# Kernel optimization log

Hardware: AMD Instinct MI355X
Metric: run time of the kernel (lower is better)

Reference implementation:

```python
import jax, jax.numpy as jnp
import numpy as np

N_NODES = 50000
N_EDGES = 800000
D_IN = 128
D_HID = 128
D_OUT = 128


def _gcn_layer(x, W, b, src, dst, norm):
    # dense projection then edge-weighted gather -> scatter-add at dst
    h = x @ W                                   # [N, d_out]
    msg = h[src] * norm[:, None]                # [E, d_out]
    out = jax.ops.segment_sum(msg, dst, num_segments=N_NODES)
    return out + b


def setup_inputs() -> dict:
    key = jax.random.key(0)
    k = jax.random.split(key, 8)
    x = jax.random.normal(k[0], (N_NODES, D_IN), dtype=jnp.float32)
    edge_index = jax.random.randint(k[1], (2, N_EDGES), 0, N_NODES, dtype=jnp.int64)
    edge_weight = jax.random.uniform(k[2], (N_EDGES,), dtype=jnp.float32)
    # GCNConv params (glorot-ish scale)
    s1 = 1.0 / np.sqrt(D_IN)
    s2 = 1.0 / np.sqrt(D_HID)
    W1 = jax.random.normal(k[3], (D_IN, D_HID), dtype=jnp.float32) * s1
    b1 = jnp.zeros((D_HID,), dtype=jnp.float32)
    W2 = jax.random.normal(k[4], (D_HID, D_OUT), dtype=jnp.float32) * s2
    b2 = jnp.zeros((D_OUT,), dtype=jnp.float32)
    return {"x": x, "edge_index": edge_index, "edge_weight": edge_weight,
            "W1": W1, "b1": b1, "W2": W2, "b2": b2}


def reference(x, edge_index, edge_weight, W1, b1, W2, b2):
    src, dst = edge_index[0], edge_index[1]
    # gcn_norm (add_self_loops=False): deg from scatter-add of edge_weight at dst
    deg = jax.ops.segment_sum(edge_weight, dst, num_segments=N_NODES)
    dinv = jnp.where(deg > 0, jax.lax.rsqrt(jnp.maximum(deg, 1e-30)), 0.0)
    norm = dinv[src] * edge_weight * dinv[dst]  # [E]
    h = jax.nn.relu(_gcn_layer(x, W1, b1, src, dst, norm))
    out = _gcn_layer(h, W2, b2, src, dst, norm)
    # F.dropout in eval mode (deterministic reference) is identity
    return out
```

## Files before the change

kernel.cpp:

```cpp
#include <hip/hip_runtime.h>

#define N_NODES 50000
#define N_EDGES 800000
#define D 128
#define MAXDEG 64
#define NBUCK 196
#define BUCKCAP 5120
#define EB1 391

typedef __attribute__((ext_vector_type(8))) short bf16x8;
typedef __attribute__((ext_vector_type(4))) float f32x4;

__device__ inline unsigned short f2bf(float f) {
    unsigned u = __float_as_uint(f);
    unsigned r = (u + 0x7fffu + ((u >> 16) & 1u)) >> 16;
    return (unsigned short)r;
}

__global__ __launch_bounds__(256) void k_bucket(const int* __restrict__ src,
                                                const int* __restrict__ dst,
                                                const float* __restrict__ ew,
                                                int* __restrict__ cursor,
                                                uint2* __restrict__ buck,
                                                const float* __restrict__ W1,
                                                const float* __restrict__ W2,
                                                unsigned short* __restrict__ Wt1,
                                                unsigned short* __restrict__ Wt2) {
    if (blockIdx.x >= EB1) {
        const float* W = (blockIdx.x == EB1) ? W1 : W2;
        unsigned short* Wt = (blockIdx.x == EB1) ? Wt1 : Wt2;
        for (int idx = threadIdx.x; idx < D * D; idx += 256) {
            int n = idx & 127, k = idx >> 7;
            Wt[n * D + k] = f2bf(W[k * D + n]);
        }
        return;
    }
    __shared__ int hist[NBUCK];
    __shared__ int base[NBUCK];
    for (int i = threadIdx.x; i < NBUCK; i += 256) hist[i] = 0;
    __syncthreads();
    int e0 = blockIdx.x * 2048 + threadIdx.x;
    int dl[8]; unsigned pay[8]; int bk[8]; bool val[8];
    #pragma unroll
    for (int j = 0; j < 8; ++j) {
        int e = e0 + j * 256;
        val[j] = e < N_EDGES;
        if (val[j]) {
            dl[j] = dst[e];
            int s = src[e];
            unsigned wf = min(__float2uint_rn(ew[e] * 65536.f), 65535u);
            pay[j] = ((unsigned)s << 16) | wf;
            bk[j] = dl[j] >> 8;
            atomicAdd(&hist[bk[j]], 1);
        }
    }
    __syncthreads();
    for (int i = threadIdx.x; i < NBUCK; i += 256) {
        int h = hist[i];
        base[i] = h ? atomicAdd(&cursor[i], h) : 0;
    }
    __syncthreads();
    for (int i = threadIdx.x; i < NBUCK; i += 256) hist[i] = 0;
    __syncthreads();
    #pragma unroll
    for (int j = 0; j < 8; ++j) {
        if (val[j]) {
            int slot = base[bk[j]] + atomicAdd(&hist[bk[j]], 1);
            if (slot < BUCKCAP)
                buck[(size_t)bk[j] * BUCKCAP + slot] = make_uint2(pay[j], dl[j] & 255);
        }
    }
}

__global__ __launch_bounds__(256) void k_build(const int* __restrict__ cursor,
                                               const uint2* __restrict__ buck,
                                               unsigned* __restrict__ csr,
                                               int* __restrict__ cnt,
                                               float* __restrict__ dinv) {
    __shared__ unsigned csr_loc[256 * MAXDEG];
    __shared__ int cnt_loc[256];
    __shared__ int deg_loc[256];
    int b = blockIdx.x;
    cnt_loc[threadIdx.x] = 0;
    deg_loc[threadIdx.x] = 0;
    __syncthreads();
    int n = min(cursor[b], BUCKCAP);
    const uint2* bb = buck + (size_t)b * BUCKCAP;
    for (int i = threadIdx.x; i < n; i += 256) {
        uint2 e = bb[i];
        int ln = e.y;
        int slot = atomicAdd(&cnt_loc[ln], 1);
        if (slot < MAXDEG) csr_loc[ln * MAXDEG + slot] = e.x;
        atomicAdd(&deg_loc[ln], (int)(e.x & 0xffffu));
    }
    __syncthreads();
    int node0 = b * 256;
    int nnodes = min(256, N_NODES - node0);
    uint4* g = (uint4*)(csr + (size_t)node0 * MAXDEG);
    const uint4* l = (const uint4*)csr_loc;
    int nv = nnodes * (MAXDEG / 4);
    for (int i = threadIdx.x; i < nv; i += 256) g[i] = l[i];
    if (threadIdx.x < nnodes) {
        int node = node0 + threadIdx.x;
        cnt[node] = min(cnt_loc[threadIdx.x], MAXDEG);
        float sum = (float)deg_loc[threadIdx.x] * (1.f / 65536.f);
        dinv[node] = sum > 0.f ? rsqrtf(fmaxf(sum, 1e-30f)) : 0.f;
    }
}

__global__ __launch_bounds__(256) void k_gemm(const void* __restrict__ Xv,
                                              const unsigned short* __restrict__ Wt,
                                              const float* __restrict__ dinv,
                                              unsigned short* __restrict__ Yb,
                                              int xIsF32) {
    __shared__ unsigned short sX[64 * D];
    int row0 = blockIdx.x * 64;
    int nr = min(64, N_NODES - row0);
    if (xIsF32) {
        const float4* xs = (const float4*)((const float*)Xv + (size_t)row0 * D);
        int nvec = nr * (D / 4);
        for (int i = threadIdx.x; i < nvec; i += 256) {
            float4 v = xs[i];
            ushort4 o;
            o.x = f2bf(v.x); o.y = f2bf(v.y); o.z = f2bf(v.z); o.w = f2bf(v.w);
            *(ushort4*)(sX + i * 4) = o;
        }
    } else {
        const uint4* xs = (const uint4*)((const unsigned short*)Xv + (size_t)row0 * D);
        int nvec = nr * (D / 8);
        for (int i = threadIdx.x; i < nvec; i += 256)
            *(uint4*)(sX + i * 8) = xs[i];
    }
    __syncthreads();

    int wave = threadIdx.x >> 6, lane = threadIdx.x & 63;
    int m = lane & 15, quad = lane >> 4;
    f32x4 acc[8];
    #pragma unroll
    for (int i = 0; i < 8; ++i) acc[i] = (f32x4){0.f, 0.f, 0.f, 0.f};

    const unsigned short* aBase = sX + (wave * 16 + m) * D + quad * 8;
    #pragma unroll
    for (int c = 0; c < 4; ++c) {
        bf16x8 a = *(const bf16x8*)(aBase + c * 32);
        #pragma unroll
        for (int n0 = 0; n0 < 8; ++n0) {
            bf16x8 b = *(const bf16x8*)(Wt + (n0 * 16 + m) * D + c * 32 + quad * 8);
            acc[n0] = __builtin_amdgcn_mfma_f32_16x16x32_bf16(a, b, acc[n0], 0, 0, 0);
        }
    }

    float dv[4];
    #pragma unroll
    for (int i = 0; i < 4; ++i) {
        int r = row0 + wave * 16 + quad * 4 + i;
        dv[i] = dinv ? (r < N_NODES ? dinv[r] : 0.f) : 1.f;
    }

    unsigned short* sOut = sX + wave * 16 * D;
    __syncthreads();
    #pragma unroll
    for (int n0 = 0; n0 < 8; ++n0)
        #pragma unroll
        for (int i = 0; i < 4; ++i)
            sOut[(quad * 4 + i) * D + n0 * 16 + m] = f2bf(acc[n0][i] * dv[i]);
    __syncthreads();
    int rr = lane >> 2, c0 = (lane & 3) * 32;
    int grow = row0 + wave * 16 + rr;
    if (grow < N_NODES) {
        uint4* dstp = (uint4*)(Yb + (size_t)grow * D + c0);
        const uint4* srcp = (const uint4*)(sOut + rr * D + c0);
        dstp[0] = srcp[0]; dstp[1] = srcp[1]; dstp[2] = srcp[2]; dstp[3] = srcp[3];
    }
}

__global__ __launch_bounds__(256) void k_aggregate(const uint4* __restrict__ H4,
                                                   const int* __restrict__ cnt,
                                                   const unsigned* __restrict__ csr,
                                                   const float* __restrict__ dinv,
                                                   const float* __restrict__ bias,
                                                   void* __restrict__ out,
                                                   int relu, int out_bf16) {
    int node = blockIdx.x * 4 + (threadIdx.x >> 6);
    int lane = threadIdx.x & 63;
    int g = lane >> 4;
    int fl = lane & 15;
    int end = min(cnt[node], MAXDEG);
    const uint4* row4 = (const uint4*)(csr + (size_t)node * MAXDEG);
    float acc[8] = {0.f, 0.f, 0.f, 0.f, 0.f, 0.f, 0.f, 0.f};
    for (int base = 0; base < end; base += 16) {
        int k0 = base + g * 4;
        if (k0 < end) {
            uint4 c4 = row4[(base >> 2) + g];
            unsigned cs[4] = {c4.x, c4.y, c4.z, c4.w};
            #pragma unroll
            for (int j = 0; j < 4; ++j) {
                if (k0 + j < end) {
                    unsigned s = cs[j] >> 16;
                    float nm = (float)(cs[j] & 0xffffu) * (1.f / 65536.f);
                    uint4 u = H4[(size_t)s * (D / 8) + fl];
                    unsigned a0[4] = {u.x, u.y, u.z, u.w};
                    #pragma unroll
                    for (int q = 0; q < 4; ++q) {
                        acc[2 * q]     += __uint_as_float(a0[q] << 16) * nm;
                        acc[2 * q + 1] += __uint_as_float(a0[q] & 0xffff0000u) * nm;
                    }
                }
            }
        }
    }
    #pragma unroll
    for (int j = 0; j < 8; ++j) {
        acc[j] += __shfl_xor(acc[j], 16, 64);
        acc[j] += __shfl_xor(acc[j], 32, 64);
    }
    if (g < 2) {
        float dn = dinv[node];
        int f = fl * 8 + g * 4;
        float v[4];
        #pragma unroll
        for (int j = 0; j < 4; ++j) {
            v[j] = acc[g * 4 + j] * dn + bias[f + j];
            if (relu) v[j] = fmaxf(v[j], 0.f);
        }
        if (out_bf16) {
            ushort4 o;
            o.x = f2bf(v[0]); o.y = f2bf(v[1]); o.z = f2bf(v[2]); o.w = f2bf(v[3]);
            *(ushort4*)((unsigned short*)out + (size_t)node * D + f) = o;
        } else {
            *(float4*)((float*)out + (size_t)node * D + f) =
                make_float4(v[0], v[1], v[2], v[3]);
        }
    }
}

extern "C" void kernel_launch(void* const* d_in, const int* in_sizes, int n_in,
                              void* d_out, int out_size, void* d_ws, size_t ws_size,
                              hipStream_t stream) {
    const float* x   = (const float*)d_in[0];
    const int*   ei  = (const int*)d_in[1];
    const float* ew  = (const float*)d_in[2];
    const float* W1  = (const float*)d_in[3];
    const float* b1  = (const float*)d_in[4];
    const float* W2  = (const float*)d_in[5];
    const float* b2  = (const float*)d_in[6];
    float* out = (float*)d_out;

    const int* src = ei;
    const int* dst = ei + N_EDGES;

    char* base = (char*)d_ws;
    size_t off = 0;
    auto take = [&](size_t bytes) -> char* {
        char* p = base + off;
        off += (bytes + 255) & ~(size_t)255;
        return p;
    };
    int*      cursor = (int*)take(NBUCK * 4);
    size_t zero_bytes = off;
    float*    dinv = (float*)take(N_NODES * 4);
    int*      cnt  = (int*)take(N_NODES * 4);
    uint2*    buck = (uint2*)take((size_t)NBUCK * BUCKCAP * 8);
    unsigned* csr  = (unsigned*)take((size_t)N_NODES * MAXDEG * 4);
    unsigned short* Wt1 = (unsigned short*)take(D * D * 2);
    unsigned short* Wt2 = (unsigned short*)take(D * D * 2);
    unsigned short* h0  = (unsigned short*)take((size_t)N_NODES * D * 2);
    unsigned short* h1  = (unsigned short*)take((size_t)N_NODES * D * 2);

    hipMemsetAsync(d_ws, 0, zero_bytes, stream);

    const int GB = (N_NODES + 63) / 64;
    const int AB = N_NODES / 4;

    k_bucket<<<EB1 + 2, 256, 0, stream>>>(src, dst, ew, cursor, buck,
                                          W1, W2, Wt1, Wt2);
    k_build<<<NBUCK, 256, 0, stream>>>(cursor, buck, csr, cnt, dinv);

    k_gemm<<<GB, 256, 0, stream>>>(x, Wt1, dinv, h0, 1);
    k_aggregate<<<AB, 256, 0, stream>>>((const uint4*)h0, cnt, csr, dinv, b1, h1, 1, 1);

    k_gemm<<<GB, 256, 0, stream>>>(h1, Wt2, dinv, h0, 0);
    k_aggregate<<<AB, 256, 0, stream>>>((const uint4*)h0, cnt, csr, dinv, b2, out, 0, 0);
}
```

Baseline: 237.8 us.

## Compact CSR and split aggregation into feature slices across blocks

The build kernel now runs a block prefix scan and claims global offsets with an atomic, writing a compacted CSR (row pointer plus count) in place of the padded 64-slot-per-node layout. The write of padding is removed and edge-list reads become contiguous. The aggregation kernel is reorganised so each block handles a 16-feature slice for 8 nodes, with 16 edges in flight per half-wave. This gives more blocks and more independent gathers per node, but each edge index is read 8 times, once per slice. The per-thread serial copy of CSR entries in the build kernel is uncoalesced.

```diff
diff --git a/kernel.cpp b/kernel.cpp
--- a/kernel.cpp
+++ b/kernel.cpp
@@ -7,6 +7,7 @@
 #define NBUCK 196
 #define BUCKCAP 5120
 #define EB1 391
+#define NSLICE 8
 
 typedef __attribute__((ext_vector_type(8))) short bf16x8;
 typedef __attribute__((ext_vector_type(4))) float f32x4;
@@ -74,19 +75,22 @@
 
 __global__ __launch_bounds__(256) void k_build(const int* __restrict__ cursor,
                                                const uint2* __restrict__ buck,
-                                               unsigned* __restrict__ csr,
-                                               int* __restrict__ cnt,
+                                               int* __restrict__ gcnt,
+                                               unsigned* __restrict__ csr_c,
+                                               int2* __restrict__ rpcnt,
                                                float* __restrict__ dinv) {
     __shared__ unsigned csr_loc[256 * MAXDEG];
     __shared__ int cnt_loc[256];
     __shared__ int deg_loc[256];
-    int b = blockIdx.x;
-    cnt_loc[threadIdx.x] = 0;
-    deg_loc[threadIdx.x] = 0;
+    __shared__ int scan[256];
+    __shared__ int baseS;
+    int b = blockIdx.x, tid = threadIdx.x;
+    cnt_loc[tid] = 0;
+    deg_loc[tid] = 0;
     __syncthreads();
     int n = min(cursor[b], BUCKCAP);
     const uint2* bb = buck + (size_t)b * BUCKCAP;
-    for (int i = threadIdx.x; i < n; i += 256) {
+    for (int i = tid; i < n; i += 256) {
         uint2 e = bb[i];
         int ln = e.y;
         int slot = atomicAdd(&cnt_loc[ln], 1);
@@ -94,17 +98,27 @@
         atomicAdd(&deg_loc[ln], (int)(e.x & 0xffffu));
     }
     __syncthreads();
+    int c = min(cnt_loc[tid], MAXDEG);
+    scan[tid] = c;
+    __syncthreads();
+    for (int off = 1; off < 256; off <<= 1) {
+        int u = tid >= off ? scan[tid - off] : 0;
+        __syncthreads();
+        scan[tid] += u;
+        __syncthreads();
+    }
+    int excl = scan[tid] - c;
+    if (tid == 255) baseS = atomicAdd(gcnt, excl + c);
+    __syncthreads();
+    int rp = baseS + excl;
     int node0 = b * 256;
     int nnodes = min(256, N_NODES - node0);
-    uint4* g = (uint4*)(csr + (size_t)node0 * MAXDEG);
-    const uint4* l = (const uint4*)csr_loc;
-    int nv = nnodes * (MAXDEG / 4);
-    for (int i = threadIdx.x; i < nv; i += 256) g[i] = l[i];
-    if (threadIdx.x < nnodes) {
-        int node = node0 + threadIdx.x;
-        cnt[node] = min(cnt_loc[threadIdx.x], MAXDEG);
-        float sum = (float)deg_loc[threadIdx.x] * (1.f / 65536.f);
+    if (tid < nnodes) {
+        int node = node0 + tid;
+        rpcnt[node] = make_int2(rp, c);
+        float sum = (float)deg_loc[tid] * (1.f / 65536.f);
         dinv[node] = sum > 0.f ? rsqrtf(fmaxf(sum, 1e-30f)) : 0.f;
+        for (int k = 0; k < c; ++k) csr_c[rp + k] = csr_loc[tid * MAXDEG + k];
     }
 }
 
@@ -174,62 +188,63 @@
     }
 }
 
-__global__ __launch_bounds__(256) void k_aggregate(const uint4* __restrict__ H4,
-                                                   const int* __restrict__ cnt,
-                                                   const unsigned* __restrict__ csr,
+__global__ __launch_bounds__(256) void k_aggregate(const unsigned short* __restrict__ H,
+                                                   const int2* __restrict__ rpcnt,
+                                                   const unsigned* __restrict__ csr_c,
                                                    const float* __restrict__ dinv,
                                                    const float* __restrict__ bias,
                                                    void* __restrict__ out,
                                                    int relu, int out_bf16) {
-    int node = blockIdx.x * 4 + (threadIdx.x >> 6);
-    int lane = threadIdx.x & 63;
-    int g = lane >> 4;
-    int fl = lane & 15;
-    int end = min(cnt[node], MAXDEG);
-    const uint4* row4 = (const uint4*)(csr + (size_t)node * MAXDEG);
+    int slice = blockIdx.x & 7;
+    int ng = blockIdx.x >> 3;
+    int half = threadIdx.x >> 5;
+    int l32 = threadIdx.x & 31;
+    int node = ng * 8 + half;
+    int2 rc = rpcnt[node];
+    int rp = rc.x, c = rc.y;
+    int f0 = slice * 16 + (l32 & 1) * 8;
     float acc[8] = {0.f, 0.f, 0.f, 0.f, 0.f, 0.f, 0.f, 0.f};
-    for (int base = 0; base < end; base += 16) {
-        int k0 = base + g * 4;
-        if (k0 < end) {
-            uint4 c4 = row4[(base >> 2) + g];
-            unsigned cs[4] = {c4.x, c4.y, c4.z, c4.w};
+    for (int base = 0; base < c; base += 16) {
+        int j = base + (l32 >> 1);
+        if (j < c) {
+            unsigned e = csr_c[rp + j];
+            unsigned s = e >> 16;
+            float w = (float)(e & 0xffffu) * (1.f / 65536.f);
+            uint4 u = *(const uint4*)(H + (size_t)s * D + f0);
+            unsigned a0[4] = {u.x, u.y, u.z, u.w};
             #pragma unroll
-            for (int j = 0; j < 4; ++j) {
-                if (k0 + j < end) {
-                    unsigned s = cs[j] >> 16;
-                    float nm = (float)(cs[j] & 0xffffu) * (1.f / 65536.f);
-                    uint4 u = H4[(size_t)s * (D / 8) + fl];
-                    unsigned a0[4] = {u.x, u.y, u.z, u.w};
-                    #pragma unroll
-                    for (int q = 0; q < 4; ++q) {
-                        acc[2 * q]     += __uint_as_float(a0[q] << 16) * nm;
-                        acc[2 * q + 1] += __uint_as_float(a0[q] & 0xffff0000u) * nm;
-                    }
-                }
+            for (int q = 0; q < 4; ++q) {
+                acc[2 * q]     += __uint_as_float(a0[q] << 16) * w;
+                acc[2 * q + 1] += __uint_as_float(a0[q] & 0xffff0000u) * w;
             }
         }
     }
     #pragma unroll
     for (int j = 0; j < 8; ++j) {
+        acc[j] += __shfl_xor(acc[j], 2, 64);
+        acc[j] += __shfl_xor(acc[j], 4, 64);
+        acc[j] += __shfl_xor(acc[j], 8, 64);
         acc[j] += __shfl_xor(acc[j], 16, 64);
-        acc[j] += __shfl_xor(acc[j], 32, 64);
-    }
-    if (g < 2) {
+    }
+    if (l32 < 2) {
         float dn = dinv[node];
-        int f = fl * 8 + g * 4;
-        float v[4];
+        float v[8];
         #pragma unroll
-        for (int j = 0; j < 4; ++j) {
-            v[j] = acc[g * 4 + j] * dn + bias[f + j];
+        for (int j = 0; j < 8; ++j) {
+            v[j] = acc[j] * dn + bias[f0 + j];
             if (relu) v[j] = fmaxf(v[j], 0.f);
         }
         if (out_bf16) {
-            ushort4 o;
-            o.x = f2bf(v[0]); o.y = f2bf(v[1]); o.z = f2bf(v[2]); o.w = f2bf(v[3]);
-            *(ushort4*)((unsigned short*)out + (size_t)node * D + f) = o;
+            ushort4 o0, o1;
+            o0.x = f2bf(v[0]); o0.y = f2bf(v[1]); o0.z = f2bf(v[2]); o0.w = f2bf(v[3]);
+            o1.x = f2bf(v[4]); o1.y = f2bf(v[5]); o1.z = f2bf(v[6]); o1.w = f2bf(v[7]);
+            unsigned short* po = (unsigned short*)out + (size_t)node * D + f0;
+            *(ushort4*)po = o0;
+            *(ushort4*)(po + 4) = o1;
         } else {
-            *(float4*)((float*)out + (size_t)node * D + f) =
-                make_float4(v[0], v[1], v[2], v[3]);
+            float* po = (float*)out + (size_t)node * D + f0;
+            *(float4*)po = make_float4(v[0], v[1], v[2], v[3]);
+            *(float4*)(po + 4) = make_float4(v[4], v[5], v[6], v[7]);
         }
     }
 }
@@ -257,11 +272,12 @@
         return p;
     };
     int*      cursor = (int*)take(NBUCK * 4);
+    int*      gcnt   = (int*)take(4);
     size_t zero_bytes = off;
-    float*    dinv = (float*)take(N_NODES * 4);
-    int*      cnt  = (int*)take(N_NODES * 4);
-    uint2*    buck = (uint2*)take((size_t)NBUCK * BUCKCAP * 8);
-    unsigned* csr  = (unsigned*)take((size_t)N_NODES * MAXDEG * 4);
+    float*    dinv   = (float*)take(N_NODES * 4);
+    int2*     rpcnt  = (int2*)take((size_t)N_NODES * 8);
+    uint2*    buck   = (uint2*)take((size_t)NBUCK * BUCKCAP * 8);
+    unsigned* csr_c  = (unsigned*)take((size_t)N_EDGES * 4);
     unsigned short* Wt1 = (unsigned short*)take(D * D * 2);
     unsigned short* Wt2 = (unsigned short*)take(D * D * 2);
     unsigned short* h0  = (unsigned short*)take((size_t)N_NODES * D * 2);
@@ -270,15 +286,15 @@
     hipMemsetAsync(d_ws, 0, zero_bytes, stream);
 
     const int GB = (N_NODES + 63) / 64;
-    const int AB = N_NODES / 4;
+    const int AB = (N_NODES / 8) * NSLICE;
 
     k_bucket<<<EB1 + 2, 256, 0, stream>>>(src, dst, ew, cursor, buck,
                                           W1, W2, Wt1, Wt2);
-    k_build<<<NBUCK, 256, 0, stream>>>(cursor, buck, csr, cnt, dinv);
+    k_build<<<NBUCK, 256, 0, stream>>>(cursor, buck, gcnt, csr_c, rpcnt, dinv);
 
     k_gemm<<<GB, 256, 0, stream>>>(x, Wt1, dinv, h0, 1);
-    k_aggregate<<<AB, 256, 0, stream>>>((const uint4*)h0, cnt, csr, dinv, b1, h1, 1, 1);
+    k_aggregate<<<AB, 256, 0, stream>>>(h0, rpcnt, csr_c, dinv, b1, h1, 1, 1);
 
     k_gemm<<<GB, 256, 0, stream>>>(h1, Wt2, dinv, h0, 0);
-    k_aggregate<<<AB, 256, 0, stream>>>((const uint4*)h0, cnt, csr, dinv, b2, out, 0, 0);
-}
+    k_aggregate<<<AB, 256, 0, stream>>>(h0, rpcnt, csr_c, dinv, b2, out, 0, 0);
+}
```

New measurement: 337.3 us. +41.8%, slower.
